# Kernel optimization log

Measured on AMD Instinct MI355X. Metric: run time of the kernel, lower is better.

The kernel has to match this reference:

```python
import jax, jax.numpy as jnp
import numpy as np

N, E = 50000, 800000
C, A_ALL, RAD_IN, FC1, FC2 = 128, 256, 32, 64, 64
H, AH, VH = 8, 16, 16  # heads, alpha channels/head, value channels/head


def _radial_mlp(x, w1, b1, w2, b2, w3, b3):
    x = jax.nn.silu(x @ w1 + b1)
    x = jax.nn.silu(x @ w2 + b2)
    return x @ w3 + b3


def _smooth_leaky_relu(x, a=0.2):
    # Equiformer SmoothLeakyReLU: 0.5*(1+a)*x + 0.5*(1-a)*x*(2*sigmoid(x)-1)
    return 0.5 * (1.0 + a) * x + 0.5 * (1.0 - a) * x * (2.0 * jax.nn.sigmoid(x) - 1.0)


def _segment_softmax(scores, seg, num_segments):
    m = jax.ops.segment_max(scores, seg, num_segments=num_segments)
    m = jnp.where(jnp.isfinite(m), m, 0.0)
    e = jnp.exp(scores - m[seg])
    s = jax.ops.segment_sum(e, seg, num_segments=num_segments)
    return e / (s[seg] + 1e-16)


def setup_inputs():
    key = jax.random.key(0)
    ks = jax.random.split(key, 16)

    def g(k, shape):
        scale = 1.0 / np.sqrt(shape[0])
        return jax.random.normal(k, shape, dtype=jnp.float32) * scale

    return {
        "node_input": jax.random.normal(ks[0], (N, C), dtype=jnp.float32),
        "node_attr": jnp.ones((N, 1), jnp.float32),
        "edge_attr": jax.random.uniform(ks[1], (E, 1), dtype=jnp.float32),
        "edge_scalars": jax.random.normal(ks[2], (E, RAD_IN), dtype=jnp.float32),
        "edge_src": jax.random.randint(ks[3], (E,), 0, N, dtype=jnp.int32),
        "edge_dst": jax.random.randint(ks[4], (E,), 0, N, dtype=jnp.int32),
        "batch": jnp.zeros((N,), jnp.int32),
        "w_src": g(ks[5], (C, C)), "b_src": jnp.zeros((C,), jnp.float32),
        "w_dst": g(ks[6], (C, C)),
        "fc_w1": g(ks[7], (RAD_IN, FC1)), "fc_b1": jnp.zeros((FC1,), jnp.float32),
        "fc_w2": g(ks[8], (FC1, FC2)), "fc_b2": jnp.zeros((FC2,), jnp.float32),
        "fc_w3": g(ks[9], (FC2, C)), "fc_b3": jnp.zeros((C,), jnp.float32),
        "w_sep": g(ks[10], (C, A_ALL)), "b_sep": jnp.zeros((A_ALL,), jnp.float32),
        "alpha_dot": jax.random.normal(ks[11], (1, H, AH), dtype=jnp.float32) * np.sqrt(2.0 / (H * AH)),
        "w_proj": g(ks[12], (H * VH, C)), "b_proj": jnp.zeros((C,), jnp.float32),
    }


def reference(node_input, node_attr, edge_attr, edge_scalars, edge_src, edge_dst, batch,
              w_src, b_src, w_dst, fc_w1, fc_b1, fc_w2, fc_b2, fc_w3, fc_b3,
              w_sep, b_sep, alpha_dot, w_proj, b_proj):
    n_nodes = node_input.shape[0]
    n_edges = edge_src.shape[0]
    # merge_src / merge_dst (LinearRS; bias only on src)
    msg_src = node_input @ w_src + b_src                     # [N, C]
    msg_dst = node_input @ w_dst                             # [N, C]
    message = msg_src[edge_src] + msg_dst[edge_dst]          # [E, C] edge gather
    # SeparableFCTP: radial-weighted depthwise tensor product (scalar irreps)
    rad_w = _radial_mlp(edge_scalars, fc_w1, fc_b1, fc_w2, fc_b2, fc_w3, fc_b3)  # [E, C]
    message = message * edge_attr * rad_w                    # depthwise TP
    message = message @ w_sep + b_sep                        # [E, A_ALL] linear to attn_all
    # Vec2AttnHeads + split alpha/value per head
    msg_h = message.reshape(n_edges, H, AH + VH)
    alpha = _smooth_leaky_relu(msg_h[:, :, :AH])             # [E, H, AH]
    value = msg_h[:, :, AH:]                                 # [E, H, VH]
    score = jnp.einsum('ehk,ahk->eh', alpha, alpha_dot)      # [E, H]
    att = _segment_softmax(score, edge_dst, n_nodes)[..., None]
    out = jax.ops.segment_sum(value * att, edge_dst, num_segments=n_nodes)  # scatter-add
    out = out.reshape(n_nodes, H * VH)                       # AttnHeads2Vec
    return out @ w_proj + b_proj
```

## Files before the change

### kernel.cpp

```cpp
#include <hip/hip_runtime.h>

#define NN 50000
#define NE 800000

typedef unsigned short u16;
typedef __bf16 bf16x8 __attribute__((ext_vector_type(8)));
typedef float f32x4 __attribute__((ext_vector_type(4)));
typedef unsigned short u16x8 __attribute__((ext_vector_type(8)));

__device__ __forceinline__ u16 f2b(float f){
  return __builtin_bit_cast(u16, (__bf16)f);
}
__device__ __forceinline__ float b2f(u16 b){
  return __uint_as_float(((unsigned)b)<<16);
}
__device__ __forceinline__ float row_sum16(float x){
  x += __int_as_float(__builtin_amdgcn_update_dpp(0, __float_as_int(x), 0x121, 0xF, 0xF, true));
  x += __int_as_float(__builtin_amdgcn_update_dpp(0, __float_as_int(x), 0x122, 0xF, 0xF, true));
  x += __int_as_float(__builtin_amdgcn_update_dpp(0, __float_as_int(x), 0x124, 0xF, 0xF, true));
  x += __int_as_float(__builtin_amdgcn_update_dpp(0, __float_as_int(x), 0x128, 0xF, 0xF, true));
  return x;
}
#define MFMA16(a,b,c) __builtin_amdgcn_mfma_f32_16x16x32_bf16((a),(b),(c),0,0,0)

__global__ void k_prep(const float* __restrict__ w1, const float* __restrict__ w2,
                       const float* __restrict__ w3, const float* __restrict__ wsep,
                       const float* __restrict__ wsrc, const float* __restrict__ wdst,
                       const float* __restrict__ wproj,
                       u16* __restrict__ w1T, u16* __restrict__ w2T,
                       u16* __restrict__ w3T, u16* __restrict__ wsepT,
                       u16* __restrict__ wsrcT, u16* __restrict__ wdstT,
                       u16* __restrict__ wprojT)
{
  int id = blockIdx.x*256 + threadIdx.x;
  if (id < 2048)  { int n=id>>5,  k=id&31;  w1T[id]   = f2b(w1[k*64+n]);    return; } id -= 2048;
  if (id < 4096)  { int n=id>>6,  k=id&63;  w2T[id]   = f2b(w2[k*64+n]);    return; } id -= 4096;
  if (id < 8192)  { int n=id>>6,  k=id&63;  w3T[id]   = f2b(w3[k*128+n]);   return; } id -= 8192;
  if (id < 32768) { int n=id>>7,  k=id&127; wsepT[id] = f2b(wsep[k*256+n]); return; } id -= 32768;
  if (id < 16384) { int n=id>>7,  k=id&127; wsrcT[id] = f2b(wsrc[k*128+n]); return; } id -= 16384;
  if (id < 16384) { int n=id>>7,  k=id&127; wdstT[id] = f2b(wdst[k*128+n]); return; } id -= 16384;
  if (id < 16384) { int n=id>>7,  k=id&127; wprojT[id]= f2b(wproj[k*128+n]); return; }
}

__global__ void k_hist(const int* __restrict__ edst, unsigned* __restrict__ cnt)
{
  int e = blockIdx.x*256 + threadIdx.x;
  if (e < NE) atomicAdd(&cnt[edst[e]], 1u);
}

__launch_bounds__(1024)
__global__ void k_scan1(const unsigned* __restrict__ cnt, unsigned* __restrict__ cur,
                        unsigned* __restrict__ btot)
{
  __shared__ unsigned wt[16];
  const int tid = threadIdx.x, lane = tid&63, w = tid>>6;
  int i = blockIdx.x*1024 + tid;
  unsigned v = (i < NN) ? cnt[i] : 0u;
  unsigned x = v;
  #pragma unroll
  for (int off=1; off<64; off<<=1){
    unsigned t = __shfl_up(x, off);
    if (lane >= off) x += t;
  }
  if (lane == 63) wt[w] = x;
  __syncthreads();
  if (w == 0){
    unsigned y = (lane < 16) ? wt[lane] : 0u;
    #pragma unroll
    for (int off=1; off<16; off<<=1){
      unsigned t = __shfl_up(y, off);
      if (lane >= off) y += t;
    }
    if (lane < 16) wt[lane] = y;
  }
  __syncthreads();
  unsigned wo = w ? wt[w-1] : 0u;
  if (i < NN) cur[i] = wo + (x - v);
  if (tid == 1023) btot[blockIdx.x] = wo + x;
}

__global__ void k_scan2(unsigned* __restrict__ btot)
{
  int lane = threadIdx.x;
  unsigned v = (lane < 49) ? btot[lane] : 0u;
  unsigned x = v;
  #pragma unroll
  for (int off=1; off<64; off<<=1){
    unsigned t = __shfl_up(x, off);
    if (lane >= off) x += t;
  }
  if (lane < 49) btot[lane] = x - v;
}

__launch_bounds__(1024)
__global__ void k_scan3(unsigned* __restrict__ cur, const unsigned* __restrict__ btot)
{
  int i = blockIdx.x*1024 + threadIdx.x;
  if (i < NN) cur[i] += btot[blockIdx.x];
}

__global__ void k_scatter(const int* __restrict__ esrc, const int* __restrict__ edst,
                          const float* __restrict__ eattr, unsigned* __restrict__ cur,
                          int4* __restrict__ ework)
{
  int e = blockIdx.x*256 + threadIdx.x;
  if (e < NE){
    int d = edst[e];
    unsigned pos = atomicAdd(&cur[d], 1u);
    ework[pos] = make_int4(e, d, esrc[e], __float_as_int(eattr[e]));
  }
}

__launch_bounds__(256)
__global__ void k_node(const float* __restrict__ x, const u16* __restrict__ wsrcT,
                       const u16* __restrict__ wdstT, const float* __restrict__ bsrc,
                       u16* __restrict__ msgsrcB, u16* __restrict__ msgdstB)
{
  __shared__ u16 sX[64*136];
  __shared__ u16 sW[128*136];
  __shared__ float sB[128];
  const int tid = threadIdx.x;
  const int n0 = blockIdx.x*64;
  for (int idx = tid; idx < 64*32; idx += 256){
    int r = idx>>5, s = idx&31;
    float4 v = make_float4(0.f,0.f,0.f,0.f);
    if (n0 + r < NN) v = *(const float4*)(x + (size_t)(n0+r)*128 + s*4);
    ushort4 o; o.x=f2b(v.x); o.y=f2b(v.y); o.z=f2b(v.z); o.w=f2b(v.w);
    *(ushort4*)(&sX[r*136 + s*4]) = o;
  }
  const int wave = tid>>6, lane = tid&63, l15 = lane&15, q = lane>>4;
  for (int half = 0; half < 2; ++half){
    const u16* wT = half ? wdstT : wsrcT;
    for (int idx = tid; idx < 128*16; idx += 256){
      int r = idx>>4, s = idx&15;
      *(uint4*)(&sW[r*136 + s*8]) = *(const uint4*)(wT + r*128 + s*8);
    }
    if (tid < 128) sB[tid] = half ? 0.0f : bsrc[tid];
    __syncthreads();
    f32x4 acc[8];
    #pragma unroll
    for (int n=0;n<8;++n) acc[n] = (f32x4){0.f,0.f,0.f,0.f};
    #pragma unroll
    for (int k0=0;k0<128;k0+=32){
      bf16x8 a = *(const bf16x8*)(&sX[(wave*16+l15)*136 + k0 + q*8]);
      #pragma unroll
      for (int n=0;n<8;++n){
        bf16x8 b = *(const bf16x8*)(&sW[(n*16+l15)*136 + k0 + q*8]);
        acc[n] = MFMA16(a,b,acc[n]);
      }
    }
    u16* outp = half ? msgdstB : msgsrcB;
    #pragma unroll
    for (int n=0;n<8;++n){
      #pragma unroll
      for (int r=0;r<4;++r){
        int row = n0 + wave*16 + q*4 + r;
        if (row < NN) outp[(size_t)row*128 + n*16 + l15] = f2b(acc[n][r] + sB[n*16+l15]);
      }
    }
    __syncthreads();
  }
}

#define PM 136
#define PH 72
#define PX 40
__launch_bounds__(256,6)
__global__ void k_edge(const float* __restrict__ escal, const int4* __restrict__ ework,
                       const u16* __restrict__ msgsrcB, const u16* __restrict__ msgdstB,
                       const u16* __restrict__ w1T, const u16* __restrict__ w2T,
                       const u16* __restrict__ w3T, const u16* __restrict__ wsepT,
                       const float* __restrict__ b1, const float* __restrict__ b2,
                       const float* __restrict__ b3, const float* __restrict__ bsep,
                       const float* __restrict__ adot,
                       float* __restrict__ num, float* __restrict__ denom)
{
  __shared__ __attribute__((aligned(16))) char pool[26624];
  u16* sH1  = (u16*)(pool + 0);
  u16* sXs  = (u16*)(pool + 9216);
  u16* sH2  = (u16*)(pool + 17408);
  u16* sMsg = (u16*)(pool + 0);

  const int tid = threadIdx.x;
  const int e0 = blockIdx.x*64;
  const int wave = tid>>6, lane = tid&63, l15 = lane&15, q = lane>>4;

  for (int j = tid; j < 512; j += 256){ int r=j>>3, s=j&7;
    int pe = ework[e0 + r].x;
    float4 v = *(const float4*)(escal + (size_t)pe*32 + s*4);
    ushort4 o; o.x=f2b(v.x); o.y=f2b(v.y); o.z=f2b(v.z); o.w=f2b(v.w);
    *(ushort4*)&sXs[r*PX + s*4] = o; }
  __syncthreads();

  {
    f32x4 acc[4];
    #pragma unroll
    for (int n=0;n<4;++n) acc[n] = (f32x4){0.f,0.f,0.f,0.f};
    bf16x8 a = *(const bf16x8*)&sXs[(wave*16+l15)*PX + q*8];
    #pragma unroll
    for (int n=0;n<4;++n){
      bf16x8 b = *(const bf16x8*)(w1T + (n*16+l15)*32 + q*8);
      acc[n] = MFMA16(a,b,acc[n]);
    }
    #pragma unroll
    for (int n=0;n<4;++n){
      float bia = b1[n*16+l15];
      #pragma unroll
      for (int r=0;r<4;++r){
        float v = acc[n][r] + bia;
        float h = v / (1.0f + __expf(-v));
        sH1[(wave*16+q*4+r)*PH + n*16+l15] = f2b(h);
      }
    }
  }
  __syncthreads();

  {
    f32x4 acc[4];
    #pragma unroll
    for (int n=0;n<4;++n) acc[n] = (f32x4){0.f,0.f,0.f,0.f};
    #pragma unroll
    for (int k0=0;k0<64;k0+=32){
      bf16x8 a = *(const bf16x8*)&sH1[(wave*16+l15)*PH + k0 + q*8];
      #pragma unroll
      for (int n=0;n<4;++n){
        bf16x8 b = *(const bf16x8*)(w2T + (n*16+l15)*64 + k0 + q*8);
        acc[n] = MFMA16(a,b,acc[n]);
      }
    }
    #pragma unroll
    for (int n=0;n<4;++n){
      float bia = b2[n*16+l15];
      #pragma unroll
      for (int r=0;r<4;++r){
        float v = acc[n][r] + bia;
        float h = v / (1.0f + __expf(-v));
        sH2[(wave*16+q*4+r)*PH + n*16+l15] = f2b(h);
      }
    }
  }
  __syncthreads();

  {
    const int m0 = (wave&1)*2, n0 = (wave>>1)*2;
    #pragma unroll
    for (int ch=0; ch<2; ++ch){
      f32x4 acc[2][2];
      #pragma unroll
      for (int mm=0;mm<2;++mm)
        #pragma unroll
        for (int nn=0;nn<2;++nn) acc[mm][nn] = (f32x4){0.f,0.f,0.f,0.f};
      const u16* w3b = w3T + (size_t)(ch*64)*64;
      #pragma unroll
      for (int k0=0;k0<64;k0+=32){
        bf16x8 a0 = *(const bf16x8*)&sH2[((m0  )*16+l15)*PH + k0 + q*8];
        bf16x8 a1 = *(const bf16x8*)&sH2[((m0+1)*16+l15)*PH + k0 + q*8];
        bf16x8 bb0 = *(const bf16x8*)(w3b + ((n0  )*16+l15)*64 + k0 + q*8);
        bf16x8 bb1 = *(const bf16x8*)(w3b + ((n0+1)*16+l15)*64 + k0 + q*8);
        acc[0][0] = MFMA16(a0,bb0,acc[0][0]);
        acc[1][0] = MFMA16(a1,bb0,acc[1][0]);
        acc[0][1] = MFMA16(a0,bb1,acc[0][1]);
        acc[1][1] = MFMA16(a1,bb1,acc[1][1]);
      }
      #pragma unroll
      for (int mm=0;mm<2;++mm){
        #pragma unroll
        for (int nn=0;nn<2;++nn){
          int c = ch*64 + (n0+nn)*16 + l15;
          float bia = b3[c];
          #pragma unroll
          for (int r=0;r<4;++r){
            float v = acc[mm][nn][r] + bia;
            sMsg[((m0+mm)*16+q*4+r)*PM + c] = f2b(v);
          }
        }
      }
    }
  }
  __syncthreads();

  for (int idx = tid; idx < 64*16; idx += 256){
    int r = idx>>4, s = idx&15;
    int cs = s*8;
    int4 em = ework[e0 + r];
    int id = em.y, is = em.z;
    float ea = __int_as_float(em.w);
    u16x8 a8 = *(const u16x8*)(msgsrcB + (size_t)is*128 + cs);
    u16x8 d8 = *(const u16x8*)(msgdstB + (size_t)id*128 + cs);
    u16x8 rw = *(const u16x8*)&sMsg[r*PM + cs];
    u16x8 o;
    #pragma unroll
    for (int j=0;j<8;++j){
      o[j] = f2b((b2f(a8[j]) + b2f(d8[j])) * ea * b2f(rw[j]));
    }
    *(u16x8*)&sMsg[r*PM + cs] = o;
  }
  __syncthreads();

  {
    const int fm0 = (wave&1)*2, fn0 = (wave>>1)*2;
    const int hh = fn0>>1;
    float* sWV = (float*)(pool + 17408);
    float* sWp = (float*)(pool + 17408 + 8704);
    const u16* wb0 = wsepT + (size_t)((fn0  )*16+l15)*128 + q*8;
    const u16* wb1 = wsepT + (size_t)((fn0+1)*16+l15)*128 + q*8;
    const int wc = tid & 31, wg = tid >> 5, wcl = wc & 15, whh = wc >> 4;
    int dreg[8];
    #pragma unroll
    for (int rr=0; rr<8; ++rr) dreg[rr] = ework[e0 + wg*8 + rr].y;

    #pragma unroll
    for (int ch=0; ch<4; ++ch){
      f32x4 acc[2][2];
      #pragma unroll
      for (int mm=0;mm<2;++mm)
        #pragma unroll
        for (int nn=0;nn<2;++nn) acc[mm][nn] = (f32x4){0.f,0.f,0.f,0.f};
      #pragma unroll
      for (int k0=0;k0<128;k0+=32){
        bf16x8 a0 = *(const bf16x8*)&sMsg[((fm0  )*16+l15)*PM + k0 + q*8];
        bf16x8 a1 = *(const bf16x8*)&sMsg[((fm0+1)*16+l15)*PM + k0 + q*8];
        bf16x8 bb0 = *(const bf16x8*)(wb0 + (size_t)ch*64*128 + k0);
        bf16x8 bb1 = *(const bf16x8*)(wb1 + (size_t)ch*64*128 + k0);
        acc[0][0] = MFMA16(a0,bb0,acc[0][0]);
        acc[1][0] = MFMA16(a1,bb0,acc[1][0]);
        acc[0][1] = MFMA16(a0,bb1,acc[0][1]);
        acc[1][1] = MFMA16(a1,bb1,acc[1][1]);
      }
      {
        const int h  = ch*2 + hh;
        const int ca = ch*64 + fn0*16;
        const float ba = bsep[ca + l15];
        const float bv = bsep[ca + 16 + l15];
        const float ad = adot[h*16 + l15];
        #pragma unroll
        for (int mm=0;mm<2;++mm){
          #pragma unroll
          for (int r=0;r<4;++r){
            float av  = acc[mm][0][r] + ba;
            float sig = 1.0f/(1.0f + __expf(-av));
            float sl  = av*(0.2f + 0.8f*sig);
            float contrib = row_sum16(sl * ad);
            float w  = __expf(contrib);
            float vv = acc[mm][1][r] + bv;
            int row  = (fm0+mm)*16 + q*4 + r;
            sWV[row*34 + hh*16 + l15] = w*vv;
            if (l15 == 0) sWp[row*2 + hh] = w;
          }
        }
      }
      __syncthreads();
      {
        const int h = ch*2 + whh;
        float av = 0.f, wa = 0.f;
        int pd = dreg[0];
        #pragma unroll
        for (int rr=0; rr<8; ++rr){
          int d = dreg[rr];
          if (d != pd){
            unsafeAtomicAdd(&num[(size_t)pd*128 + h*16 + wcl], av);
            if (wcl == 0) unsafeAtomicAdd(&denom[(size_t)pd*8 + h], wa);
            av = 0.f; wa = 0.f; pd = d;
          }
          int row = wg*8 + rr;
          av += sWV[row*34 + wc];
          if (wcl == 0) wa += sWp[row*2 + whh];
        }
        unsafeAtomicAdd(&num[(size_t)pd*128 + h*16 + wcl], av);
        if (wcl == 0) unsafeAtomicAdd(&denom[(size_t)pd*8 + h], wa);
      }
      __syncthreads();
    }
  }
}

__launch_bounds__(256)
__global__ void k_out(const float* __restrict__ num, const float* __restrict__ denom,
                      const u16* __restrict__ wprojT, const float* __restrict__ bproj,
                      float* __restrict__ out)
{
  __shared__ u16 sX[64*136];
  __shared__ u16 sW[128*136];
  __shared__ float sB[128];
  const int tid = threadIdx.x;
  const int n0 = blockIdx.x*64;
  for (int idx = tid; idx < 64*128; idx += 256){
    int r = idx>>7, c = idx&127;
    float xv = 0.f;
    int row = n0 + r;
    if (row < NN){
      float d = denom[row*8 + (c>>4)];
      xv = num[(size_t)row*128 + c] / (d + 1e-16f);
    }
    sX[r*136 + c] = f2b(xv);
  }
  for (int idx = tid; idx < 128*16; idx += 256){ int r=idx>>4, s=idx&15;
    *(uint4*)&sW[r*136 + s*8] = *(const uint4*)(wprojT + r*128 + s*8); }
  if (tid < 128) sB[tid] = bproj[tid];
  __syncthreads();
  const int wave = tid>>6, lane = tid&63, l15 = lane&15, q = lane>>4;
  f32x4 acc[8];
  #pragma unroll
  for (int n=0;n<8;++n) acc[n] = (f32x4){0.f,0.f,0.f,0.f};
  #pragma unroll
  for (int k0=0;k0<128;k0+=32){
    bf16x8 a = *(const bf16x8*)&sX[(wave*16+l15)*136 + k0 + q*8];
    #pragma unroll
    for (int n=0;n<8;++n){
      bf16x8 b = *(const bf16x8*)&sW[(n*16+l15)*136 + k0 + q*8];
      acc[n] = MFMA16(a,b,acc[n]);
    }
  }
  #pragma unroll
  for (int n=0;n<8;++n){
    #pragma unroll
    for (int r=0;r<4;++r){
      int row = n0 + wave*16 + q*4 + r;
      if (row < NN) out[(size_t)row*128 + n*16 + l15] = acc[n][r] + sB[n*16+l15];
    }
  }
}

extern "C" void kernel_launch(void* const* d_in, const int* in_sizes, int n_in,
                              void* d_out, int out_size, void* d_ws, size_t ws_size,
                              hipStream_t stream)
{
  const float* node_input = (const float*)d_in[0];
  const float* eattr = (const float*)d_in[2];
  const float* escal = (const float*)d_in[3];
  const int*   esrc  = (const int*)d_in[4];
  const int*   edst  = (const int*)d_in[5];
  const float* wsrc  = (const float*)d_in[7];
  const float* bsrc  = (const float*)d_in[8];
  const float* wdst  = (const float*)d_in[9];
  const float* w1    = (const float*)d_in[10];
  const float* b1    = (const float*)d_in[11];
  const float* w2    = (const float*)d_in[12];
  const float* b2    = (const float*)d_in[13];
  const float* w3    = (const float*)d_in[14];
  const float* b3    = (const float*)d_in[15];
  const float* wsep  = (const float*)d_in[16];
  const float* bsep  = (const float*)d_in[17];
  const float* adot  = (const float*)d_in[18];
  const float* wproj = (const float*)d_in[19];
  const float* bproj = (const float*)d_in[20];

  char* ws = (char*)d_ws;
  size_t off = 0;
  auto alloc = [&](size_t bytes)->void*{ void* p = ws + off; off += (bytes + 255) & ~(size_t)255; return p; };
  u16*   msgsrcB = (u16*)alloc((size_t)NN*128*2);
  u16*   msgdstB = (u16*)alloc((size_t)NN*128*2);
  float* num     = (float*)alloc((size_t)NN*128*4);
  float* denom   = (float*)alloc((size_t)NN*8*4);
  u16* w1T    = (u16*)alloc(2048*2);
  u16* w2T    = (u16*)alloc(4096*2);
  u16* w3T    = (u16*)alloc(8192*2);
  u16* wsepT  = (u16*)alloc(32768*2);
  u16* wsrcT  = (u16*)alloc(16384*2);
  u16* wdstT  = (u16*)alloc(16384*2);
  u16* wprojT = (u16*)alloc(16384*2);
  unsigned* cnt = (unsigned*)alloc((size_t)NN*4);
  unsigned* cur = (unsigned*)alloc((size_t)NN*4);
  unsigned* btot = (unsigned*)alloc(64*4);
  int4*  ework  = (int4*)alloc((size_t)NE*16);

  hipMemsetAsync(num,   0, (size_t)NN*128*4, stream);
  hipMemsetAsync(denom, 0, (size_t)NN*8*4,   stream);
  hipMemsetAsync(cnt,   0, (size_t)NN*4,     stream);

  k_prep<<<376, 256, 0, stream>>>(w1,w2,w3,wsep,wsrc,wdst,wproj,
                                  w1T,w2T,w3T,wsepT,wsrcT,wdstT,wprojT);
  k_hist<<<3125, 256, 0, stream>>>(edst, cnt);
  k_scan1<<<49, 1024, 0, stream>>>(cnt, cur, btot);
  k_scan2<<<1, 64, 0, stream>>>(btot);
  k_scan3<<<49, 1024, 0, stream>>>(cur, btot);
  k_scatter<<<3125, 256, 0, stream>>>(esrc, edst, eattr, cur, ework);
  k_node<<<782, 256, 0, stream>>>(node_input, wsrcT, wdstT, bsrc, msgsrcB, msgdstB);
  k_edge<<<12500, 256, 0, stream>>>(escal, ework, msgsrcB, msgdstB,
                                    w1T, w2T, w3T, wsepT, b1, b2, b3, bsep, adot,
                                    num, denom);
  k_out<<<782, 256, 0, stream>>>(num, denom, wprojT, bproj, (float*)d_out);
}
```

Before: 757.1 us.

## Scatter attention atomics directly from MFMA registers and fold scan3 into scatter

```diff
diff --git a/kernel.cpp b/kernel.cpp
--- a/kernel.cpp
+++ b/kernel.cpp
@@ -92,21 +92,14 @@
   if (lane < 49) btot[lane] = x - v;
 }
 
-__launch_bounds__(1024)
-__global__ void k_scan3(unsigned* __restrict__ cur, const unsigned* __restrict__ btot)
-{
-  int i = blockIdx.x*1024 + threadIdx.x;
-  if (i < NN) cur[i] += btot[blockIdx.x];
-}
-
 __global__ void k_scatter(const int* __restrict__ esrc, const int* __restrict__ edst,
                           const float* __restrict__ eattr, unsigned* __restrict__ cur,
-                          int4* __restrict__ ework)
+                          const unsigned* __restrict__ btot, int4* __restrict__ ework)
 {
   int e = blockIdx.x*256 + threadIdx.x;
   if (e < NE){
     int d = edst[e];
-    unsigned pos = atomicAdd(&cur[d], 1u);
+    unsigned pos = btot[d>>10] + atomicAdd(&cur[d], 1u);
     ework[pos] = make_int4(e, d, esrc[e], __float_as_int(eattr[e]));
   }
 }
@@ -300,14 +293,14 @@
   {
     const int fm0 = (wave&1)*2, fn0 = (wave>>1)*2;
     const int hh = fn0>>1;
-    float* sWV = (float*)(pool + 17408);
-    float* sWp = (float*)(pool + 17408 + 8704);
     const u16* wb0 = wsepT + (size_t)((fn0  )*16+l15)*128 + q*8;
     const u16* wb1 = wsepT + (size_t)((fn0+1)*16+l15)*128 + q*8;
-    const int wc = tid & 31, wg = tid >> 5, wcl = wc & 15, whh = wc >> 4;
-    int dreg[8];
-    #pragma unroll
-    for (int rr=0; rr<8; ++rr) dreg[rr] = ework[e0 + wg*8 + rr].y;
+    int dq[2][4];
+    #pragma unroll
+    for (int mm=0;mm<2;++mm)
+      #pragma unroll
+      for (int r=0;r<4;++r)
+        dq[mm][r] = ework[e0 + (fm0+mm)*16 + q*4 + r].y;
 
     #pragma unroll
     for (int ch=0; ch<4; ++ch){
@@ -335,6 +328,8 @@
         const float ad = adot[h*16 + l15];
         #pragma unroll
         for (int mm=0;mm<2;++mm){
+          float avac = 0.f, waac = 0.f;
+          int pd = dq[mm][0];
           #pragma unroll
           for (int r=0;r<4;++r){
             float av  = acc[mm][0][r] + ba;
@@ -343,31 +338,18 @@
             float contrib = row_sum16(sl * ad);
             float w  = __expf(contrib);
             float vv = acc[mm][1][r] + bv;
-            int row  = (fm0+mm)*16 + q*4 + r;
-            sWV[row*34 + hh*16 + l15] = w*vv;
-            if (l15 == 0) sWp[row*2 + hh] = w;
+            int d = dq[mm][r];
+            if (d != pd){
+              unsafeAtomicAdd(&num[(size_t)pd*128 + h*16 + l15], avac);
+              if (l15 == 0) unsafeAtomicAdd(&denom[(size_t)pd*8 + h], waac);
+              avac = 0.f; waac = 0.f; pd = d;
+            }
+            avac += w*vv;
+            waac += w;
           }
+          unsafeAtomicAdd(&num[(size_t)pd*128 + h*16 + l15], avac);
+          if (l15 == 0) unsafeAtomicAdd(&denom[(size_t)pd*8 + h], waac);
         }
-      }
-      __syncthreads();
-      {
-        const int h = ch*2 + whh;
-        float av = 0.f, wa = 0.f;
-        int pd = dreg[0];
-        #pragma unroll
-        for (int rr=0; rr<8; ++rr){
-          int d = dreg[rr];
-          if (d != pd){
-            unsafeAtomicAdd(&num[(size_t)pd*128 + h*16 + wcl], av);
-            if (wcl == 0) unsafeAtomicAdd(&denom[(size_t)pd*8 + h], wa);
-            av = 0.f; wa = 0.f; pd = d;
-          }
-          int row = wg*8 + rr;
-          av += sWV[row*34 + wc];
-          if (wcl == 0) wa += sWp[row*2 + whh];
-        }
-        unsafeAtomicAdd(&num[(size_t)pd*128 + h*16 + wcl], av);
-        if (wcl == 0) unsafeAtomicAdd(&denom[(size_t)pd*8 + h], wa);
       }
       __syncthreads();
     }
@@ -473,8 +455,7 @@
   k_hist<<<3125, 256, 0, stream>>>(edst, cnt);
   k_scan1<<<49, 1024, 0, stream>>>(cnt, cur, btot);
   k_scan2<<<1, 64, 0, stream>>>(btot);
-  k_scan3<<<49, 1024, 0, stream>>>(cur, btot);
-  k_scatter<<<3125, 256, 0, stream>>>(esrc, edst, eattr, cur, ework);
+  k_scatter<<<3125, 256, 0, stream>>>(esrc, edst, eattr, cur, btot, ework);
   k_node<<<782, 256, 0, stream>>>(node_input, wsrcT, wdstT, bsrc, msgsrcB, msgdstB);
   k_edge<<<12500, 256, 0, stream>>>(escal, ework, msgsrcB, msgdstB,
                                     w1T, w2T, w3T, wsepT, b1, b2, b3, bsep, adot,
```

Result: slower. 773.4 us (+2.2%).

## Merge setup kernels, read weights from global, prefetch edge gathers

Applied to the files above, without the earlier changes.

```diff
diff --git a/kernel.cpp b/kernel.cpp
--- a/kernel.cpp
+++ b/kernel.cpp
@@ -23,28 +23,28 @@
 }
 #define MFMA16(a,b,c) __builtin_amdgcn_mfma_f32_16x16x32_bf16((a),(b),(c),0,0,0)
 
-__global__ void k_prep(const float* __restrict__ w1, const float* __restrict__ w2,
-                       const float* __restrict__ w3, const float* __restrict__ wsep,
-                       const float* __restrict__ wsrc, const float* __restrict__ wdst,
-                       const float* __restrict__ wproj,
-                       u16* __restrict__ w1T, u16* __restrict__ w2T,
-                       u16* __restrict__ w3T, u16* __restrict__ wsepT,
-                       u16* __restrict__ wsrcT, u16* __restrict__ wdstT,
-                       u16* __restrict__ wprojT)
-{
-  int id = blockIdx.x*256 + threadIdx.x;
-  if (id < 2048)  { int n=id>>5,  k=id&31;  w1T[id]   = f2b(w1[k*64+n]);    return; } id -= 2048;
-  if (id < 4096)  { int n=id>>6,  k=id&63;  w2T[id]   = f2b(w2[k*64+n]);    return; } id -= 4096;
-  if (id < 8192)  { int n=id>>6,  k=id&63;  w3T[id]   = f2b(w3[k*128+n]);   return; } id -= 8192;
-  if (id < 32768) { int n=id>>7,  k=id&127; wsepT[id] = f2b(wsep[k*256+n]); return; } id -= 32768;
-  if (id < 16384) { int n=id>>7,  k=id&127; wsrcT[id] = f2b(wsrc[k*128+n]); return; } id -= 16384;
-  if (id < 16384) { int n=id>>7,  k=id&127; wdstT[id] = f2b(wdst[k*128+n]); return; } id -= 16384;
-  if (id < 16384) { int n=id>>7,  k=id&127; wprojT[id]= f2b(wproj[k*128+n]); return; }
-}
-
-__global__ void k_hist(const int* __restrict__ edst, unsigned* __restrict__ cnt)
-{
-  int e = blockIdx.x*256 + threadIdx.x;
+__global__ void k_prep_hist(const float* __restrict__ w1, const float* __restrict__ w2,
+                            const float* __restrict__ w3, const float* __restrict__ wsep,
+                            const float* __restrict__ wsrc, const float* __restrict__ wdst,
+                            const float* __restrict__ wproj,
+                            u16* __restrict__ w1T, u16* __restrict__ w2T,
+                            u16* __restrict__ w3T, u16* __restrict__ wsepT,
+                            u16* __restrict__ wsrcT, u16* __restrict__ wdstT,
+                            u16* __restrict__ wprojT,
+                            const int* __restrict__ edst, unsigned* __restrict__ cnt)
+{
+  if (blockIdx.x < 376){
+    int id = blockIdx.x*256 + threadIdx.x;
+    if (id < 2048)  { int n=id>>5,  k=id&31;  w1T[id]   = f2b(w1[k*64+n]);    return; } id -= 2048;
+    if (id < 4096)  { int n=id>>6,  k=id&63;  w2T[id]   = f2b(w2[k*64+n]);    return; } id -= 4096;
+    if (id < 8192)  { int n=id>>6,  k=id&63;  w3T[id]   = f2b(w3[k*128+n]);   return; } id -= 8192;
+    if (id < 32768) { int n=id>>7,  k=id&127; wsepT[id] = f2b(wsep[k*256+n]); return; } id -= 32768;
+    if (id < 16384) { int n=id>>7,  k=id&127; wsrcT[id] = f2b(wsrc[k*128+n]); return; } id -= 16384;
+    if (id < 16384) { int n=id>>7,  k=id&127; wdstT[id] = f2b(wdst[k*128+n]); return; } id -= 16384;
+    if (id < 16384) { int n=id>>7,  k=id&127; wprojT[id]= f2b(wproj[k*128+n]); return; }
+    return;
+  }
+  int e = (blockIdx.x - 376)*256 + threadIdx.x;
   if (e < NE) atomicAdd(&cnt[edst[e]], 1u);
 }
 
@@ -92,35 +92,26 @@
   if (lane < 49) btot[lane] = x - v;
 }
 
-__launch_bounds__(1024)
-__global__ void k_scan3(unsigned* __restrict__ cur, const unsigned* __restrict__ btot)
-{
-  int i = blockIdx.x*1024 + threadIdx.x;
-  if (i < NN) cur[i] += btot[blockIdx.x];
-}
-
-__global__ void k_scatter(const int* __restrict__ esrc, const int* __restrict__ edst,
-                          const float* __restrict__ eattr, unsigned* __restrict__ cur,
-                          int4* __restrict__ ework)
-{
-  int e = blockIdx.x*256 + threadIdx.x;
-  if (e < NE){
-    int d = edst[e];
-    unsigned pos = atomicAdd(&cur[d], 1u);
-    ework[pos] = make_int4(e, d, esrc[e], __float_as_int(eattr[e]));
-  }
-}
-
 __launch_bounds__(256)
-__global__ void k_node(const float* __restrict__ x, const u16* __restrict__ wsrcT,
-                       const u16* __restrict__ wdstT, const float* __restrict__ bsrc,
-                       u16* __restrict__ msgsrcB, u16* __restrict__ msgdstB)
+__global__ void k_scatter_node(const int* __restrict__ esrc, const int* __restrict__ edst,
+                               const float* __restrict__ eattr, unsigned* __restrict__ cur,
+                               const unsigned* __restrict__ btot, int4* __restrict__ ework,
+                               const float* __restrict__ x, const u16* __restrict__ wsrcT,
+                               const u16* __restrict__ wdstT, const float* __restrict__ bsrc,
+                               u16* __restrict__ msgsrcB, u16* __restrict__ msgdstB)
 {
   __shared__ u16 sX[64*136];
-  __shared__ u16 sW[128*136];
-  __shared__ float sB[128];
   const int tid = threadIdx.x;
-  const int n0 = blockIdx.x*64;
+  if (blockIdx.x < 3125){
+    int e = blockIdx.x*256 + tid;
+    if (e < NE){
+      int d = edst[e];
+      unsigned pos = btot[d>>10] + atomicAdd(&cur[d], 1u);
+      ework[pos] = make_int4(e, d, esrc[e], __float_as_int(eattr[e]));
+    }
+    return;
+  }
+  const int n0 = (blockIdx.x - 3125)*64;
   for (int idx = tid; idx < 64*32; idx += 256){
     int r = idx>>5, s = idx&31;
     float4 v = make_float4(0.f,0.f,0.f,0.f);
@@ -128,15 +119,10 @@
     ushort4 o; o.x=f2b(v.x); o.y=f2b(v.y); o.z=f2b(v.z); o.w=f2b(v.w);
     *(ushort4*)(&sX[r*136 + s*4]) = o;
   }
+  __syncthreads();
   const int wave = tid>>6, lane = tid&63, l15 = lane&15, q = lane>>4;
   for (int half = 0; half < 2; ++half){
     const u16* wT = half ? wdstT : wsrcT;
-    for (int idx = tid; idx < 128*16; idx += 256){
-      int r = idx>>4, s = idx&15;
-      *(uint4*)(&sW[r*136 + s*8]) = *(const uint4*)(wT + r*128 + s*8);
-    }
-    if (tid < 128) sB[tid] = half ? 0.0f : bsrc[tid];
-    __syncthreads();
     f32x4 acc[8];
     #pragma unroll
     for (int n=0;n<8;++n) acc[n] = (f32x4){0.f,0.f,0.f,0.f};
@@ -145,20 +131,20 @@
       bf16x8 a = *(const bf16x8*)(&sX[(wave*16+l15)*136 + k0 + q*8]);
       #pragma unroll
       for (int n=0;n<8;++n){
-        bf16x8 b = *(const bf16x8*)(&sW[(n*16+l15)*136 + k0 + q*8]);
+        bf16x8 b = *(const bf16x8*)(wT + (n*16+l15)*128 + k0 + q*8);
         acc[n] = MFMA16(a,b,acc[n]);
       }
     }
     u16* outp = half ? msgdstB : msgsrcB;
     #pragma unroll
     for (int n=0;n<8;++n){
+      float bia = half ? 0.0f : bsrc[n*16+l15];
       #pragma unroll
       for (int r=0;r<4;++r){
         int row = n0 + wave*16 + q*4 + r;
-        if (row < NN) outp[(size_t)row*128 + n*16 + l15] = f2b(acc[n][r] + sB[n*16+l15]);
-      }
-    }
-    __syncthreads();
+        if (row < NN) outp[(size_t)row*128 + n*16 + l15] = f2b(acc[n][r] + bia);
+      }
+    }
   }
 }
 
@@ -185,6 +171,19 @@
   const int e0 = blockIdx.x*64;
   const int wave = tid>>6, lane = tid&63, l15 = lane&15, q = lane>>4;
 
+  u16x8 pf[4];
+  int   pid[4];
+  float pea[4];
+  #pragma unroll
+  for (int t=0;t<4;++t){
+    int idx = tid + t*256;
+    int r = idx>>4, s = idx&15;
+    int4 em = ework[e0 + r];
+    pf[t]  = *(const u16x8*)(msgsrcB + (size_t)em.z*128 + s*8);
+    pid[t] = em.y;
+    pea[t] = __int_as_float(em.w);
+  }
+
   for (int j = tid; j < 512; j += 256){ int r=j>>3, s=j&7;
     int pe = ework[e0 + r].x;
     float4 v = *(const float4*)(escal + (size_t)pe*32 + s*4);
@@ -279,19 +278,18 @@
   }
   __syncthreads();
 
-  for (int idx = tid; idx < 64*16; idx += 256){
+  #pragma unroll
+  for (int t=0;t<4;++t){
+    int idx = tid + t*256;
     int r = idx>>4, s = idx&15;
     int cs = s*8;
-    int4 em = ework[e0 + r];
-    int id = em.y, is = em.z;
-    float ea = __int_as_float(em.w);
-    u16x8 a8 = *(const u16x8*)(msgsrcB + (size_t)is*128 + cs);
-    u16x8 d8 = *(const u16x8*)(msgdstB + (size_t)id*128 + cs);
+    u16x8 d8 = *(const u16x8*)(msgdstB + (size_t)pid[t]*128 + cs);
+    float ea = pea[t];
     u16x8 rw = *(const u16x8*)&sMsg[r*PM + cs];
     u16x8 o;
     #pragma unroll
     for (int j=0;j<8;++j){
-      o[j] = f2b((b2f(a8[j]) + b2f(d8[j])) * ea * b2f(rw[j]));
+      o[j] = f2b((b2f(pf[t][j]) + b2f(d8[j])) * ea * b2f(rw[j]));
     }
     *(u16x8*)&sMsg[r*PM + cs] = o;
   }
@@ -380,8 +378,6 @@
                       float* __restrict__ out)
 {
   __shared__ u16 sX[64*136];
-  __shared__ u16 sW[128*136];
-  __shared__ float sB[128];
   const int tid = threadIdx.x;
   const int n0 = blockIdx.x*64;
   for (int idx = tid; idx < 64*128; idx += 256){
@@ -394,9 +390,6 @@
     }
     sX[r*136 + c] = f2b(xv);
   }
-  for (int idx = tid; idx < 128*16; idx += 256){ int r=idx>>4, s=idx&15;
-    *(uint4*)&sW[r*136 + s*8] = *(const uint4*)(wprojT + r*128 + s*8); }
-  if (tid < 128) sB[tid] = bproj[tid];
   __syncthreads();
   const int wave = tid>>6, lane = tid&63, l15 = lane&15, q = lane>>4;
   f32x4 acc[8];
@@ -407,16 +400,17 @@
     bf16x8 a = *(const bf16x8*)&sX[(wave*16+l15)*136 + k0 + q*8];
     #pragma unroll
     for (int n=0;n<8;++n){
-      bf16x8 b = *(const bf16x8*)&sW[(n*16+l15)*136 + k0 + q*8];
+      bf16x8 b = *(const bf16x8*)(wprojT + (n*16+l15)*128 + k0 + q*8);
       acc[n] = MFMA16(a,b,acc[n]);
     }
   }
   #pragma unroll
   for (int n=0;n<8;++n){
+    float bia = bproj[n*16+l15];
     #pragma unroll
     for (int r=0;r<4;++r){
       int row = n0 + wave*16 + q*4 + r;
-      if (row < NN) out[(size_t)row*128 + n*16 + l15] = acc[n][r] + sB[n*16+l15];
+      if (row < NN) out[(size_t)row*128 + n*16 + l15] = acc[n][r] + bia;
     }
   }
 }
@@ -468,14 +462,14 @@
   hipMemsetAsync(denom, 0, (size_t)NN*8*4,   stream);
   hipMemsetAsync(cnt,   0, (size_t)NN*4,     stream);
 
-  k_prep<<<376, 256, 0, stream>>>(w1,w2,w3,wsep,wsrc,wdst,wproj,
-                                  w1T,w2T,w3T,wsepT,wsrcT,wdstT,wprojT);
-  k_hist<<<3125, 256, 0, stream>>>(edst, cnt);
+  k_prep_hist<<<3501, 256, 0, stream>>>(w1,w2,w3,wsep,wsrc,wdst,wproj,
+                                        w1T,w2T,w3T,wsepT,wsrcT,wdstT,wprojT,
+                                        edst, cnt);
   k_scan1<<<49, 1024, 0, stream>>>(cnt, cur, btot);
   k_scan2<<<1, 64, 0, stream>>>(btot);
-  k_scan3<<<49, 1024, 0, stream>>>(cur, btot);
-  k_scatter<<<3125, 256, 0, stream>>>(esrc, edst, eattr, cur, ework);
-  k_node<<<782, 256, 0, stream>>>(node_input, wsrcT, wdstT, bsrc, msgsrcB, msgdstB);
+  k_scatter_node<<<3907, 256, 0, stream>>>(esrc, edst, eattr, cur, btot, ework,
+                                           node_input, wsrcT, wdstT, bsrc,
+                                           msgsrcB, msgdstB);
   k_edge<<<12500, 256, 0, stream>>>(escal, ework, msgsrcB, msgdstB,
                                     w1T, w2T, w3T, wsepT, b1, b2, b3, bsep, adot,
                                     num, denom);
```

Measured after the change: 828.7 us. 1.09x slower.
